# Kernel optimization log

Hardware: AMD Instinct MI355X
Metric: run time of the kernel (lower is better)

## Reference

```python
import jax, jax.numpy as jnp
import numpy as np

N, FIN, F, H = 4096, 128, 64, 8
NEG = -1e10


def setup_inputs() -> dict:
    key = jax.random.key(0)
    ks = jax.random.split(key, 6)
    X = jax.random.normal(ks[0], (N, FIN), dtype=jnp.float32)
    # sparse-ish binary adjacency with self loops, stored dense (as the layer expects)
    A = (jax.random.uniform(ks[1], (N, N)) < 0.05).astype(jnp.int32)
    A = A.at[jnp.arange(N), jnp.arange(N)].set(1)
    W = jax.random.normal(ks[2], (H, FIN, F), dtype=jnp.float32) * (1.0 / np.sqrt(FIN))
    b = jnp.zeros((H, F), dtype=jnp.float32)
    a_self = jax.random.normal(ks[3], (H, F), dtype=jnp.float32) * (1.0 / np.sqrt(F))
    a_neigh = jax.random.normal(ks[4], (H, F), dtype=jnp.float32) * (1.0 / np.sqrt(F))
    return {"X": X, "A": A, "W": W, "b": b, "a_self": a_self, "a_neigh": a_neigh}


def reference(X, A, W, b, a_self, a_neigh):
    # Dropout layers run in inference mode in the original call -> identity.
    feats = jnp.einsum('nf,hfo->hno', X, W)              # [H, N, F]
    s_self = jnp.einsum('hno,ho->hn', feats, a_self)     # [H, N]
    s_neigh = jnp.einsum('hno,ho->hn', feats, a_neigh)   # [H, N]
    scores = s_self[:, :, None] + s_neigh[:, None, :]    # [H, N, N]
    scores = jnp.where(scores > 0, scores, 0.2 * scores)  # LeakyReLU(0.2)
    mask = (1.0 - A.astype(jnp.float32)) * NEG            # [N, N]
    attn = jax.nn.softmax(scores + mask[None], axis=-1)   # [H, N, N]
    out = jnp.einsum('hnm,hmo->hno', attn, feats) + b[:, None, :]
    out = jax.nn.elu(out)                                 # [H, N, F]
    # concat heads -> [N, H*F]
    return jnp.transpose(out, (1, 0, 2)).reshape(N, H * F)
```

## Files before the change

kernel.cpp:

```cpp
#include <hip/hip_runtime.h>
#include <cmath>


#define NN 4096
#define FIN 128
#define FF 64
#define HH 8

typedef _Float16 h2 __attribute__((ext_vector_type(2)));
typedef _Float16 h4 __attribute__((ext_vector_type(4)));
typedef _Float16 h8 __attribute__((ext_vector_type(8)));
typedef float f32x2 __attribute__((ext_vector_type(2)));
typedef float f32x4 __attribute__((ext_vector_type(4)));

union H8 {
  h8 v;
  h2 p[4];
};
union H4 {
  h4 v;
  h2 p[2];
};

static __device__ __forceinline__ void gload16(const void* g, void* l) {
  __builtin_amdgcn_global_load_lds(
      (const __attribute__((address_space(1))) unsigned int*)g,
      (__attribute__((address_space(3))) unsigned int*)l, 16, 0, 0);
}

__global__ __launch_bounds__(256) void pack_kernel(
    const int* __restrict__ A, const float* __restrict__ W,
    const float* __restrict__ X, unsigned long long* __restrict__ bits,
    _Float16* __restrict__ Wsw, _Float16* __restrict__ Xsw) {
  const int b = blockIdx.x;
  const int tid = threadIdx.x;
  const int wave = tid >> 6, lane = tid & 63;
  if (b < NN) {
    __shared__ int ldsT[4][4][256];
    const int* ar = A + (size_t)b * NN;
    int4 v[4];
#pragma unroll
    for (int it = 0; it < 4; ++it) {
      const int g = wave * 4 + it;
      v[it] = *(const int4*)(ar + g * 256 + lane * 4);
    }
#pragma unroll
    for (int it = 0; it < 4; ++it) *(int4*)&ldsT[wave][it][lane * 4] = v[it];
    unsigned long long* br = bits + ((size_t)b << 6);
#pragma unroll
    for (int it = 0; it < 4; ++it) {
      const int g = wave * 4 + it;
      int w0 = ldsT[wave][it][0 * 64 + lane];
      int w1 = ldsT[wave][it][1 * 64 + lane];
      int w2 = ldsT[wave][it][2 * 64 + lane];
      int w3 = ldsT[wave][it][3 * 64 + lane];
      unsigned long long m0 = __ballot(w0 != 0);
      unsigned long long m1 = __ballot(w1 != 0);
      unsigned long long m2 = __ballot(w2 != 0);
      unsigned long long m3 = __ballot(w3 != 0);
      if (lane == 0) {
        ulonglong2 p0 = {m0, m1}, p1 = {m2, m3};
        *(ulonglong2*)(br + g * 4 + 0) = p0;
        *(ulonglong2*)(br + g * 4 + 2) = p1;
      }
    }
  } else if (b < NN + 2) {
    const int h0 = (b - NN) * 4;
    for (int h = h0; h < h0 + 4; ++h) {
      for (int c = tid; c < 1024; c += 256) {
        int ln = c & 63, nb = (c >> 6) & 3, kt = c >> 8;
        int f = nb * 16 + (ln & 15);
        int k0 = kt * 32 + (ln >> 4) * 8;
        h8 v;
#pragma unroll
        for (int j = 0; j < 8; ++j)
          v[j] = (_Float16)W[((size_t)(h * FIN) + k0 + j) * FF + f];
        *(h8*)(Wsw + ((size_t)(((h * 4 + kt) * 4 + nb) * 64 + ln)) * 8) = v;
      }
    }
  } else {
    const int tile = (b - NN - 2) * 4 + wave;
    const int l16 = lane & 15, quad = lane >> 4;
    const float* xr = X + (size_t)(tile * 16 + l16) * FIN;
#pragma unroll
    for (int kt = 0; kt < 4; ++kt) {
      int k0 = kt * 32 + quad * 8;
      f32x4 x0 = *(const f32x4*)(xr + k0);
      f32x4 x1 = *(const f32x4*)(xr + k0 + 4);
      h8 v = {(_Float16)x0[0], (_Float16)x0[1], (_Float16)x0[2],
              (_Float16)x0[3], (_Float16)x1[0], (_Float16)x1[1],
              (_Float16)x1[2], (_Float16)x1[3]};
      *(h8*)(Xsw + ((size_t)((tile * 4 + kt) * 64 + lane)) * 8) = v;
    }
  }
}

__global__ __launch_bounds__(256) void feats_kernel(
    const _Float16* __restrict__ Xsw, const _Float16* __restrict__ Wsw,
    const float* __restrict__ a_self, const float* __restrict__ a_neigh,
    _Float16* __restrict__ feats_sw, _Float16* __restrict__ es_h,
    _Float16* __restrict__ esn_h, _Float16* __restrict__ et_h,
    _Float16* __restrict__ etn_h) {
  const int h = blockIdx.y;
  const int tid = threadIdx.x, wave = tid >> 6, lane = tid & 63;
  const int l16 = lane & 15, quad = lane >> 4;
  const int rt = blockIdx.x * 4 + wave;
  const int r0 = rt * 16;

  f32x4 acc[4];
#pragma unroll
  for (int nb = 0; nb < 4; ++nb) acc[nb] = (f32x4){0.f, 0.f, 0.f, 0.f};

  const _Float16* xp = Xsw + ((size_t)(rt * 4) * 64 + lane) * 8;
  const _Float16* wp = Wsw + ((size_t)(h * 16) * 64 + lane) * 8;
  h8 Af[4];
#pragma unroll
  for (int kt = 0; kt < 4; ++kt) Af[kt] = *(const h8*)(xp + kt * 512);
#pragma unroll
  for (int kt = 0; kt < 4; ++kt)
#pragma unroll
    for (int nb = 0; nb < 4; ++nb) {
      h8 Bf = *(const h8*)(wp + (kt * 4 + nb) * 512);
      acc[nb] = __builtin_amdgcn_mfma_f32_16x16x32_f16(Af[kt], Bf, acc[nb], 0, 0, 0);
    }

  float as[4], an[4];
#pragma unroll
  for (int nb = 0; nb < 4; ++nb) {
    as[nb] = a_self[h * FF + nb * 16 + l16];
    an[nb] = a_neigh[h * FF + nb * 16 + l16];
  }
#pragma unroll
  for (int r = 0; r < 4; ++r) {
    float ps = acc[0][r] * as[0] + acc[1][r] * as[1] + acc[2][r] * as[2] +
               acc[3][r] * as[3];
    float pn = acc[0][r] * an[0] + acc[1][r] * an[1] + acc[2][r] * an[2] +
               acc[3][r] * an[3];
#pragma unroll
    for (int m = 1; m <= 8; m <<= 1) {
      ps += __shfl_xor(ps, m, 64);
      pn += __shfl_xor(pn, m, 64);
    }
    if (l16 == 0) {
      int node = h * NN + r0 + quad * 4 + r;
      es_h[node] = (_Float16)__expf(ps - 2.0f);
      esn_h[node] = (_Float16)__expf(0.2f * ps - 2.0f);
      et_h[node] = (_Float16)__expf(pn - 2.0f);
      etn_h[node] = (_Float16)__expf(0.2f * pn - 2.0f);
    }
  }

  const int kb = r0 >> 5;
  const int quadA = ((r0 >> 4) & 1) * 2 + (quad >> 1);
  const int jbase = (quad & 1) << 2;
#pragma unroll
  for (int nb = 0; nb < 4; ++nb) {
    h4 v = {(_Float16)acc[nb][0], (_Float16)acc[nb][1], (_Float16)acc[nb][2],
            (_Float16)acc[nb][3]};
    size_t off = ((size_t)((h * 128 + kb) * 4 + nb) << 9) +
                 ((quadA * 16 + l16) << 3) + jbase;
    *(h4*)(feats_sw + off) = v;
  }
}

__global__ __launch_bounds__(512, 4) void attn_kernel(
    const unsigned long long* __restrict__ Abits,
    const _Float16* __restrict__ feats_sw, const _Float16* __restrict__ es_h,
    const _Float16* __restrict__ esn_h, const _Float16* __restrict__ et_h,
    const _Float16* __restrict__ etn_h, const float* __restrict__ bias,
    float* __restrict__ out) {
  const int bid = blockIdx.x;
  const int h = bid & 7, n0 = (bid >> 3) << 6;
  const int tid = threadIdx.x, wave = tid >> 6, lane = tid & 63;
  const int l16 = lane & 15, quad = lane >> 4;
  const int rh = wave & 1, ctw = (wave >> 1) & 1, kfw = wave >> 2;
  const int shTot = (kfw << 5) + (quad << 3);

  __shared__ __align__(16) char smem[3 * 19456];
  __shared__ h4 lutS[16];

  if (tid < 16) {
    h4 m;
#pragma unroll
    for (int j = 0; j < 4; ++j) m[j] = (_Float16)((tid >> j) & 1);
    lutS[tid] = m;
  }
  __syncthreads();

  h2 esp[2], esnp[2];
#pragma unroll
  for (int rt = 0; rt < 2; ++rt) {
    const int myrow = n0 + (rh << 5) + (rt << 4) + l16;
    _Float16 e = es_h[h * NN + myrow];
    _Float16 en = esn_h[h * NN + myrow];
    esp[rt] = (h2){e, e};
    esnp[rt] = (h2){en, en};
  }

  f32x4 acc[2][4], accd[2];
#pragma unroll
  for (int rt = 0; rt < 2; ++rt) {
    accd[rt] = (f32x4){0.f, 0.f, 0.f, 0.f};
#pragma unroll
    for (int nb = 0; nb < 4; ++nb) acc[rt][nb] = (f32x4){0.f, 0.f, 0.f, 0.f};
  }
  const h8 ONES = {(_Float16)1.f, (_Float16)1.f, (_Float16)1.f, (_Float16)1.f,
                   (_Float16)1.f, (_Float16)1.f, (_Float16)1.f, (_Float16)1.f};

  const char* gF = (const char*)feats_sw + ((size_t)h << 19);
  const char* gE = (const char*)et_h + (h << 13);
  const char* gEN = (const char*)etn_h + (h << 13);
  const char* gB = (const char*)Abits + ((size_t)n0 << 9);

#define STAGE(s_, Lp_)                                                         \
  do {                                                                         \
    char* L_ = (char*)(Lp_);                                                   \
    const char* src_ = gF + ((size_t)(s_) << 14) + (wave << 11) + (lane << 4); \
    gload16(src_, L_ + (wave << 11) + (lane << 4));                            \
    gload16(src_ + 1024, L_ + (wave << 11) + 1024 + (lane << 4));              \
    if (wave == 0)                                                             \
      gload16(gE + ((s_) << 8) + (l16 << 4), L_ + 16384 + (lane << 4));        \
    if (wave == 1)                                                             \
      gload16(gEN + ((s_) << 8) + (l16 << 4), L_ + 17408 + (lane << 4));       \
    if (wave == 2)                                                             \
      gload16(gB + ((size_t)lane << 9) + ((s_) << 4), L_ + 18432 + (lane << 4)); \
  } while (0)

#define ITER(s_, SL, NSL, dostage_, last_)                                     \
  {                                                                            \
    __builtin_amdgcn_sched_barrier(0);                                         \
    if (last_) {                                                               \
      asm volatile("s_waitcnt vmcnt(0)" ::: "memory");                         \
    } else if (wave < 3) {                                                     \
      asm volatile("s_waitcnt vmcnt(3)" ::: "memory");                         \
    } else {                                                                   \
      asm volatile("s_waitcnt vmcnt(2)" ::: "memory");                         \
    }                                                                          \
    __builtin_amdgcn_sched_barrier(0);                                         \
    __builtin_amdgcn_s_barrier();                                              \
    if (dostage_) STAGE((s_) + 2, smem + (NSL)*19456);                         \
    const char* L = smem + (SL)*19456;                                         \
    unsigned long long mb0 = *(const unsigned long long*)(                     \
        L + 18432 + (((rh << 5) + l16) << 4) + (ctw << 3));                    \
    unsigned long long mb1 = *(const unsigned long long*)(                     \
        L + 18432 + (((rh << 5) + 16 + l16) << 4) + (ctw << 3));               \
    H8 ET, ETN;                                                                \
    ET.v = *(const h8*)(L + 16384 + (ctw << 7) + (kfw << 6) + (quad << 4));    \
    ETN.v = *(const h8*)(L + 17408 + (ctw << 7) + (kfw << 6) + (quad << 4));   \
    const char* fB = L + (ctw << 13) + (kfw << 12) + (lane << 4);              \
    h8 B0 = *(const h8*)(fB);                                                  \
    h8 B1 = *(const h8*)(fB + 1024);                                           \
    h8 B2 = *(const h8*)(fB + 2048);                                           \
    h8 B3 = *(const h8*)(fB + 3072);                                           \
    _Pragma("unroll") for (int rt = 0; rt < 2; ++rt) {                         \
      const unsigned byt = (unsigned)((rt ? mb1 : mb0) >> shTot) & 0xFFu;      \
      H4 mlo, mhi;                                                             \
      mlo.v = lutS[byt & 15u];                                                 \
      mhi.v = lutS[byt >> 4];                                                  \
      H8 P;                                                                    \
      _Pragma("unroll") for (int p = 0; p < 4; ++p) {                          \
        h2 a_ = esp[rt] * ET.p[p];                                             \
        h2 b_ = esnp[rt] * ETN.p[p];                                           \
        h2 r_ = __builtin_elementwise_max(a_, b_);                             \
        P.p[p] = r_ * (p < 2 ? mlo.p[p] : mhi.p[p - 2]);                       \
      }                                                                        \
      __builtin_amdgcn_s_setprio(1);                                           \
      acc[rt][0] =                                                             \
          __builtin_amdgcn_mfma_f32_16x16x32_f16(P.v, B0, acc[rt][0], 0, 0, 0);\
      acc[rt][1] =                                                             \
          __builtin_amdgcn_mfma_f32_16x16x32_f16(P.v, B1, acc[rt][1], 0, 0, 0);\
      acc[rt][2] =                                                             \
          __builtin_amdgcn_mfma_f32_16x16x32_f16(P.v, B2, acc[rt][2], 0, 0, 0);\
      acc[rt][3] =                                                             \
          __builtin_amdgcn_mfma_f32_16x16x32_f16(P.v, B3, acc[rt][3], 0, 0, 0);\
      accd[rt] =                                                               \
          __builtin_amdgcn_mfma_f32_16x16x32_f16(P.v, ONES, accd[rt], 0, 0, 0);\
      __builtin_amdgcn_s_setprio(0);                                           \
    }                                                                          \
  }

  STAGE(0, smem);
  STAGE(1, smem + 19456);

  for (int sb = 0; sb < 30; sb += 3) {
    ITER(sb + 0, 0, 2, 1, 0);
    ITER(sb + 1, 1, 0, 1, 0);
    ITER(sb + 2, 2, 1, 1, 0);
  }
  ITER(30, 0, 2, 0, 0);
  ITER(31, 1, 0, 0, 1);
#undef ITER
#undef STAGE

  float(*accL)[16][68] = (float(*)[16][68])smem;
  float* denL = (float*)(smem + 8 * 16 * 68 * 4);
  const int erow = tid >> 4;
  const int rh_o = erow >> 4, r16 = erow & 15;
  const int ec0 = (tid & 15) << 2;
#pragma unroll
  for (int rt = 0; rt < 2; ++rt) {
    __syncthreads();
#pragma unroll
    for (int nb = 0; nb < 4; ++nb)
#pragma unroll
      for (int r = 0; r < 4; ++r)
        accL[wave][quad * 4 + r][nb * 16 + l16] = acc[rt][nb][r];
    if (l16 == 0) {
#pragma unroll
      for (int r = 0; r < 4; ++r) denL[wave * 16 + quad * 4 + r] = accd[rt][r];
    }
    __syncthreads();
    f32x4 v = (f32x4){0.f, 0.f, 0.f, 0.f};
    float dn = 0.f;
#pragma unroll
    for (int cw = 0; cw < 4; ++cw) {
      const int w = rh_o + ((cw & 1) << 1) + ((cw >> 1) << 2);
      v += *(const f32x4*)&accL[w][r16][ec0];
      dn += denL[w * 16 + r16];
    }
    float inv = 1.0f / dn;
    const f32x4 bv = *(const f32x4*)(bias + h * FF + ec0);
#pragma unroll
    for (int i = 0; i < 4; ++i) {
      float x = v[i] * inv + bv[i];
      v[i] = x > 0.f ? x : (__expf(x) - 1.0f);
    }
    *(f32x4*)(out + (size_t)(n0 + (rh_o << 5) + (rt << 4) + r16) * (HH * FF) +
              h * FF + ec0) = v;
  }
}

extern "C" void kernel_launch(void* const* d_in, const int* in_sizes, int n_in,
                              void* d_out, int out_size, void* d_ws,
                              size_t ws_size, hipStream_t stream) {
  const float* X = (const float*)d_in[0];
  const int* A = (const int*)d_in[1];
  const float* W = (const float*)d_in[2];
  const float* b = (const float*)d_in[3];
  const float* a_self = (const float*)d_in[4];
  const float* a_neigh = (const float*)d_in[5];
  float* out = (float*)d_out;

  char* ws = (char*)d_ws;
  unsigned long long* Abits = (unsigned long long*)ws;
  _Float16* feats_sw = (_Float16*)(ws + (2u << 20));
  _Float16* es_h = (_Float16*)(ws + (6u << 20));
  _Float16* esn_h = (_Float16*)(ws + (6u << 20) + (64u << 10));
  _Float16* et_h = (_Float16*)(ws + (6u << 20) + (128u << 10));
  _Float16* etn_h = (_Float16*)(ws + (6u << 20) + (192u << 10));
  _Float16* Wsw = (_Float16*)(ws + (6u << 20) + (256u << 10));
  _Float16* Xsw = (_Float16*)(ws + (6u << 20) + (384u << 10));

  pack_kernel<<<NN + 66, 256, 0, stream>>>(A, W, X, Abits, Wsw, Xsw);
  feats_kernel<<<dim3(64, 8), 256, 0, stream>>>(Xsw, Wsw, a_self, a_neigh,
                                                feats_sw, es_h, esn_h, et_h,
                                                etn_h);
  attn_kernel<<<512, 512, 0, stream>>>(Abits, feats_sw, es_h, esn_h, et_h,
                                       etn_h, b, out);
}
```

Measured before the change: 142.0 us.

## Widen attention k-tile, give each wave all 64 rows, replace denominator MFMA with fdot2

The attention kernel now has each wave cover all 64 rows (four row tiles) over a quarter of the column chunk, and each stage doubles to 256 neighbour columns. So every B fragment loaded from LDS feeds four row tiles instead of two, with half as many iterations and barriers. The denominator MFMA against a ones vector is replaced by per-lane fdot2 accumulations plus cross-quad shuffles, removing one MFMA per row tile. The pipeline drops from triple to double buffering with a full vmcnt(0) wait each iteration, which may expose global load latency. The larger accumulator set also raises register pressure at 512 threads per block.

```diff
diff --git a/kernel.cpp b/kernel.cpp
--- a/kernel.cpp
+++ b/kernel.cpp
@@ -21,6 +21,15 @@
   h4 v;
   h2 p[2];
 };
+
+static __device__ __forceinline__ float dot2acc(h2 a, float c) {
+#if __has_builtin(__builtin_amdgcn_fdot2)
+  return __builtin_amdgcn_fdot2(a, (h2){(_Float16)1.f, (_Float16)1.f}, c,
+                                false);
+#else
+  return c + (float)a[0] + (float)a[1];
+#endif
+}
 
 static __device__ __forceinline__ void gload16(const void* g, void* l) {
   __builtin_amdgcn_global_load_lds(
@@ -173,10 +182,10 @@
   const int h = bid & 7, n0 = (bid >> 3) << 6;
   const int tid = threadIdx.x, wave = tid >> 6, lane = tid & 63;
   const int l16 = lane & 15, quad = lane >> 4;
-  const int rh = wave & 1, ctw = (wave >> 1) & 1, kfw = wave >> 2;
-  const int shTot = (kfw << 5) + (quad << 3);
-
-  __shared__ __align__(16) char smem[3 * 19456];
+  const int ctw = wave & 3, kfw = wave >> 2;
+  const int shq = quad << 3;
+
+  __shared__ __align__(16) char smem[2 * 36864];
   __shared__ h4 lutS[16];
 
   if (tid < 16) {
@@ -187,73 +196,70 @@
   }
   __syncthreads();
 
-  h2 esp[2], esnp[2];
-#pragma unroll
-  for (int rt = 0; rt < 2; ++rt) {
-    const int myrow = n0 + (rh << 5) + (rt << 4) + l16;
+  h2 esp[4], esnp[4];
+#pragma unroll
+  for (int rt = 0; rt < 4; ++rt) {
+    const int myrow = n0 + (rt << 4) + l16;
     _Float16 e = es_h[h * NN + myrow];
     _Float16 en = esn_h[h * NN + myrow];
     esp[rt] = (h2){e, e};
     esnp[rt] = (h2){en, en};
   }
 
-  f32x4 acc[2][4], accd[2];
-#pragma unroll
-  for (int rt = 0; rt < 2; ++rt) {
-    accd[rt] = (f32x4){0.f, 0.f, 0.f, 0.f};
+  f32x4 acc[4][4];
+  float dsA[4] = {0.f, 0.f, 0.f, 0.f}, dsB[4] = {0.f, 0.f, 0.f, 0.f};
+#pragma unroll
+  for (int rt = 0; rt < 4; ++rt)
 #pragma unroll
     for (int nb = 0; nb < 4; ++nb) acc[rt][nb] = (f32x4){0.f, 0.f, 0.f, 0.f};
-  }
-  const h8 ONES = {(_Float16)1.f, (_Float16)1.f, (_Float16)1.f, (_Float16)1.f,
-                   (_Float16)1.f, (_Float16)1.f, (_Float16)1.f, (_Float16)1.f};
 
   const char* gF = (const char*)feats_sw + ((size_t)h << 19);
   const char* gE = (const char*)et_h + (h << 13);
   const char* gEN = (const char*)etn_h + (h << 13);
   const char* gB = (const char*)Abits + ((size_t)n0 << 9);
 
+  const unsigned fO = (wave << 12) + (lane << 4);
+
 #define STAGE(s_, Lp_)                                                         \
   do {                                                                         \
     char* L_ = (char*)(Lp_);                                                   \
-    const char* src_ = gF + ((size_t)(s_) << 14) + (wave << 11) + (lane << 4); \
-    gload16(src_, L_ + (wave << 11) + (lane << 4));                            \
-    gload16(src_ + 1024, L_ + (wave << 11) + 1024 + (lane << 4));              \
+    const char* sf_ = gF + ((size_t)(s_) << 15) + fO;                          \
+    _Pragma("unroll") for (int i = 0; i < 4; ++i)                              \
+        gload16(sf_ + (i << 10), L_ + fO + (i << 10));                         \
     if (wave == 0)                                                             \
-      gload16(gE + ((s_) << 8) + (l16 << 4), L_ + 16384 + (lane << 4));        \
+      gload16(gE + ((s_) << 9) + (lane << 4), L_ + 32768 + (lane << 4));       \
     if (wave == 1)                                                             \
-      gload16(gEN + ((s_) << 8) + (l16 << 4), L_ + 17408 + (lane << 4));       \
+      gload16(gEN + ((s_) << 9) + (lane << 4), L_ + 33792 + (lane << 4));      \
     if (wave == 2)                                                             \
-      gload16(gB + ((size_t)lane << 9) + ((s_) << 4), L_ + 18432 + (lane << 4)); \
+      gload16(gB + ((size_t)(lane >> 1) << 9) + ((s_) << 5) +                  \
+                  ((lane & 1) << 4),                                           \
+              L_ + 34816 + (lane << 4));                                       \
+    if (wave == 3)                                                             \
+      gload16(gB + ((size_t)((lane >> 1) + 32) << 9) + ((s_) << 5) +           \
+                  ((lane & 1) << 4),                                           \
+              L_ + 35840 + (lane << 4));                                       \
   } while (0)
 
-#define ITER(s_, SL, NSL, dostage_, last_)                                     \
+#define ITER(s_, SL, dostage_)                                                 \
   {                                                                            \
     __builtin_amdgcn_sched_barrier(0);                                         \
-    if (last_) {                                                               \
-      asm volatile("s_waitcnt vmcnt(0)" ::: "memory");                         \
-    } else if (wave < 3) {                                                     \
-      asm volatile("s_waitcnt vmcnt(3)" ::: "memory");                         \
-    } else {                                                                   \
-      asm volatile("s_waitcnt vmcnt(2)" ::: "memory");                         \
-    }                                                                          \
+    asm volatile("s_waitcnt vmcnt(0)" ::: "memory");                           \
     __builtin_amdgcn_sched_barrier(0);                                         \
     __builtin_amdgcn_s_barrier();                                              \
-    if (dostage_) STAGE((s_) + 2, smem + (NSL)*19456);                         \
-    const char* L = smem + (SL)*19456;                                         \
-    unsigned long long mb0 = *(const unsigned long long*)(                     \
-        L + 18432 + (((rh << 5) + l16) << 4) + (ctw << 3));                    \
-    unsigned long long mb1 = *(const unsigned long long*)(                     \
-        L + 18432 + (((rh << 5) + 16 + l16) << 4) + (ctw << 3));               \
+    if (dostage_) STAGE((s_) + 1, smem + (1 - (SL)) * 36864);                  \
+    const char* L = smem + (SL)*36864;                                         \
     H8 ET, ETN;                                                                \
-    ET.v = *(const h8*)(L + 16384 + (ctw << 7) + (kfw << 6) + (quad << 4));    \
-    ETN.v = *(const h8*)(L + 17408 + (ctw << 7) + (kfw << 6) + (quad << 4));   \
+    ET.v = *(const h8*)(L + 32768 + (ctw << 7) + (kfw << 6) + (quad << 4));    \
+    ETN.v = *(const h8*)(L + 33792 + (ctw << 7) + (kfw << 6) + (quad << 4));   \
     const char* fB = L + (ctw << 13) + (kfw << 12) + (lane << 4);              \
     h8 B0 = *(const h8*)(fB);                                                  \
     h8 B1 = *(const h8*)(fB + 1024);                                           \
     h8 B2 = *(const h8*)(fB + 2048);                                           \
     h8 B3 = *(const h8*)(fB + 3072);                                           \
-    _Pragma("unroll") for (int rt = 0; rt < 2; ++rt) {                         \
-      const unsigned byt = (unsigned)((rt ? mb1 : mb0) >> shTot) & 0xFFu;      \
+    _Pragma("unroll") for (int rt = 0; rt < 4; ++rt) {                         \
+      const unsigned w32 = *(const unsigned*)(                                 \
+          L + 34816 + (((rt << 4) + l16) << 5) + (ctw << 3) + (kfw << 2));     \
+      const unsigned byt = (w32 >> shq) & 0xFFu;                               \
       H4 mlo, mhi;                                                             \
       mlo.v = lutS[byt & 15u];                                                 \
       mhi.v = lutS[byt >> 4];                                                  \
@@ -262,7 +268,12 @@
         h2 a_ = esp[rt] * ET.p[p];                                             \
         h2 b_ = esnp[rt] * ETN.p[p];                                           \
         h2 r_ = __builtin_elementwise_max(a_, b_);                             \
-        P.p[p] = r_ * (p < 2 ? mlo.p[p] : mhi.p[p - 2]);                       \
+        h2 pm_ = r_ * (p < 2 ? mlo.p[p] : mhi.p[p - 2]);                       \
+        P.p[p] = pm_;                                                          \
+        if (p & 1)                                                             \
+          dsB[rt] = dot2acc(pm_, dsB[rt]);                                     \
+        else                                                                   \
+          dsA[rt] = dot2acc(pm_, dsA[rt]);                                     \
       }                                                                        \
       __builtin_amdgcn_s_setprio(1);                                           \
       acc[rt][0] =                                                             \
@@ -273,60 +284,65 @@
           __builtin_amdgcn_mfma_f32_16x16x32_f16(P.v, B2, acc[rt][2], 0, 0, 0);\
       acc[rt][3] =                                                             \
           __builtin_amdgcn_mfma_f32_16x16x32_f16(P.v, B3, acc[rt][3], 0, 0, 0);\
-      accd[rt] =                                                               \
-          __builtin_amdgcn_mfma_f32_16x16x32_f16(P.v, ONES, accd[rt], 0, 0, 0);\
       __builtin_amdgcn_s_setprio(0);                                           \
     }                                                                          \
   }
 
   STAGE(0, smem);
-  STAGE(1, smem + 19456);
-
-  for (int sb = 0; sb < 30; sb += 3) {
-    ITER(sb + 0, 0, 2, 1, 0);
-    ITER(sb + 1, 1, 0, 1, 0);
-    ITER(sb + 2, 2, 1, 1, 0);
-  }
-  ITER(30, 0, 2, 0, 0);
-  ITER(31, 1, 0, 0, 1);
+
+  for (int sb = 0; sb < 14; sb += 2) {
+    ITER(sb + 0, 0, 1);
+    ITER(sb + 1, 1, 1);
+  }
+  ITER(14, 0, 1);
+  ITER(15, 1, 0);
 #undef ITER
 #undef STAGE
 
-  float(*accL)[16][68] = (float(*)[16][68])smem;
-  float* denL = (float*)(smem + 8 * 16 * 68 * 4);
-  const int erow = tid >> 4;
-  const int rh_o = erow >> 4, r16 = erow & 15;
-  const int ec0 = (tid & 15) << 2;
-#pragma unroll
-  for (int rt = 0; rt < 2; ++rt) {
+  float den[4];
+#pragma unroll
+  for (int rt = 0; rt < 4; ++rt) {
+    float d = dsA[rt] + dsB[rt];
+    d += __shfl_xor(d, 16, 64);
+    d += __shfl_xor(d, 32, 64);
+    den[rt] = d;
+  }
+
+  float(*accL)[32][68] = (float(*)[32][68])smem;
+  float* denL = (float*)(smem + 8 * 32 * 68 * 4);
+  const int rr = tid >> 4, ec0 = (tid & 15) << 2;
+  const f32x4 bv = *(const f32x4*)(bias + h * FF + ec0);
+#pragma unroll
+  for (int ph = 0; ph < 2; ++ph) {
     __syncthreads();
 #pragma unroll
-    for (int nb = 0; nb < 4; ++nb)
-#pragma unroll
-      for (int r = 0; r < 4; ++r)
-        accL[wave][quad * 4 + r][nb * 16 + l16] = acc[rt][nb][r];
-    if (l16 == 0) {
-#pragma unroll
-      for (int r = 0; r < 4; ++r) denL[wave * 16 + quad * 4 + r] = accd[rt][r];
+    for (int r2 = 0; r2 < 2; ++r2) {
+      const int rt = ph * 2 + r2;
+#pragma unroll
+      for (int nb = 0; nb < 4; ++nb)
+#pragma unroll
+        for (int r = 0; r < 4; ++r)
+          accL[wave][(r2 << 4) + (quad << 2) + r][(nb << 4) + l16] =
+              acc[rt][nb][r];
+      if (quad == 0) denL[(wave << 5) + (r2 << 4) + l16] = den[rt];
     }
     __syncthreads();
     f32x4 v = (f32x4){0.f, 0.f, 0.f, 0.f};
     float dn = 0.f;
 #pragma unroll
-    for (int cw = 0; cw < 4; ++cw) {
-      const int w = rh_o + ((cw & 1) << 1) + ((cw >> 1) << 2);
-      v += *(const f32x4*)&accL[w][r16][ec0];
-      dn += denL[w * 16 + r16];
+    for (int w = 0; w < 8; ++w) {
+      v += *(const f32x4*)&accL[w][rr][ec0];
+      dn += denL[(w << 5) + rr];
     }
     float inv = 1.0f / dn;
-    const f32x4 bv = *(const f32x4*)(bias + h * FF + ec0);
+    f32x4 o;
 #pragma unroll
     for (int i = 0; i < 4; ++i) {
       float x = v[i] * inv + bv[i];
-      v[i] = x > 0.f ? x : (__expf(x) - 1.0f);
-    }
-    *(f32x4*)(out + (size_t)(n0 + (rh_o << 5) + (rt << 4) + r16) * (HH * FF) +
-              h * FF + ec0) = v;
+      o[i] = x > 0.f ? x : (__expf(x) - 1.0f);
+    }
+    *(f32x4*)(out + (size_t)(n0 + (ph << 5) + rr) * (HH * FF) + h * FF + ec0) =
+        o;
   }
 }
 
```

Result: slower. 184.6 us (+30.0%).

## Double rows per attention block and compute softmax denominators with dot2

Applied to the files above, without the earlier changes.

Each attention block now handles 128 rows instead of 64, so every staged feats tile from LDS feeds twice as many MFMAs, and the grid is halved to 256 blocks. The denominator MFMA against a ones vector is replaced by fdot2 accumulation on the VALU plus cross-quad shuffles. The LUT-based mask expansion is replaced by bitfield-extract and perm masking. The cost is more accumulator registers (launch bounds lowered to 2 blocks per CU) and only 256 blocks, which may leave some of the GPU's CUs idle.

```diff
diff --git a/kernel.cpp b/kernel.cpp
--- a/kernel.cpp
+++ b/kernel.cpp
@@ -17,10 +17,31 @@
   h8 v;
   h2 p[4];
 };
-union H4 {
-  h4 v;
-  h2 p[2];
+union U2 {
+  h2 h;
+  unsigned u;
 };
+
+static __device__ __forceinline__ float dot2acc(h2 a, float c) {
+#if __has_builtin(__builtin_amdgcn_fdot2)
+  return __builtin_amdgcn_fdot2(a, (h2){(_Float16)1.f, (_Float16)1.f}, c,
+                                false);
+#else
+  return c + (float)a[0] + (float)a[1];
+#endif
+}
+
+static __device__ __forceinline__ unsigned mask2(unsigned w, int j) {
+#if __has_builtin(__builtin_amdgcn_sbfe) && __has_builtin(__builtin_amdgcn_perm)
+  int lo = __builtin_amdgcn_sbfe((int)w, j, 1);
+  int hi = __builtin_amdgcn_sbfe((int)w, j + 1, 1);
+  return __builtin_amdgcn_perm((unsigned)hi, (unsigned)lo, 0x05040100u);
+#else
+  int lo = ((int)(w << (31 - j))) >> 31;
+  int hi = ((int)(w << (30 - j))) >> 31;
+  return ((unsigned)lo & 0xFFFFu) | ((unsigned)hi << 16);
+#endif
+}
 
 static __device__ __forceinline__ void gload16(const void* g, void* l) {
   __builtin_amdgcn_global_load_lds(
@@ -163,49 +184,37 @@
   }
 }
 
-__global__ __launch_bounds__(512, 4) void attn_kernel(
+__global__ __launch_bounds__(512, 2) void attn_kernel(
     const unsigned long long* __restrict__ Abits,
     const _Float16* __restrict__ feats_sw, const _Float16* __restrict__ es_h,
     const _Float16* __restrict__ esn_h, const _Float16* __restrict__ et_h,
     const _Float16* __restrict__ etn_h, const float* __restrict__ bias,
     float* __restrict__ out) {
   const int bid = blockIdx.x;
-  const int h = bid & 7, n0 = (bid >> 3) << 6;
+  const int h = bid & 7, n0 = (bid >> 3) << 7;
   const int tid = threadIdx.x, wave = tid >> 6, lane = tid & 63;
   const int l16 = lane & 15, quad = lane >> 4;
   const int rh = wave & 1, ctw = (wave >> 1) & 1, kfw = wave >> 2;
-  const int shTot = (kfw << 5) + (quad << 3);
-
-  __shared__ __align__(16) char smem[3 * 19456];
-  __shared__ h4 lutS[16];
-
-  if (tid < 16) {
-    h4 m;
-#pragma unroll
-    for (int j = 0; j < 4; ++j) m[j] = (_Float16)((tid >> j) & 1);
-    lutS[tid] = m;
-  }
-  __syncthreads();
-
-  h2 esp[2], esnp[2];
-#pragma unroll
-  for (int rt = 0; rt < 2; ++rt) {
-    const int myrow = n0 + (rh << 5) + (rt << 4) + l16;
+  const int shq = quad << 3;
+
+  __shared__ __align__(16) char smem[3 * 20480];
+
+  h2 esp[4], esnp[4];
+#pragma unroll
+  for (int rt = 0; rt < 4; ++rt) {
+    const int myrow = n0 + (rh << 6) + (rt << 4) + l16;
     _Float16 e = es_h[h * NN + myrow];
     _Float16 en = esn_h[h * NN + myrow];
     esp[rt] = (h2){e, e};
     esnp[rt] = (h2){en, en};
   }
 
-  f32x4 acc[2][4], accd[2];
-#pragma unroll
-  for (int rt = 0; rt < 2; ++rt) {
-    accd[rt] = (f32x4){0.f, 0.f, 0.f, 0.f};
+  f32x4 acc[4][4];
+  float dsA[4] = {0.f, 0.f, 0.f, 0.f}, dsB[4] = {0.f, 0.f, 0.f, 0.f};
+#pragma unroll
+  for (int rt = 0; rt < 4; ++rt)
 #pragma unroll
     for (int nb = 0; nb < 4; ++nb) acc[rt][nb] = (f32x4){0.f, 0.f, 0.f, 0.f};
-  }
-  const h8 ONES = {(_Float16)1.f, (_Float16)1.f, (_Float16)1.f, (_Float16)1.f,
-                   (_Float16)1.f, (_Float16)1.f, (_Float16)1.f, (_Float16)1.f};
 
   const char* gF = (const char*)feats_sw + ((size_t)h << 19);
   const char* gE = (const char*)et_h + (h << 13);
@@ -224,6 +233,9 @@
       gload16(gEN + ((s_) << 8) + (l16 << 4), L_ + 17408 + (lane << 4));       \
     if (wave == 2)                                                             \
       gload16(gB + ((size_t)lane << 9) + ((s_) << 4), L_ + 18432 + (lane << 4)); \
+    if (wave == 3)                                                             \
+      gload16(gB + ((size_t)(64 + lane) << 9) + ((s_) << 4),                   \
+              L_ + 19456 + (lane << 4));                                       \
   } while (0)
 
 #define ITER(s_, SL, NSL, dostage_, last_)                                     \
@@ -231,19 +243,15 @@
     __builtin_amdgcn_sched_barrier(0);                                         \
     if (last_) {                                                               \
       asm volatile("s_waitcnt vmcnt(0)" ::: "memory");                         \
-    } else if (wave < 3) {                                                     \
+    } else if (wave < 4) {                                                     \
       asm volatile("s_waitcnt vmcnt(3)" ::: "memory");                         \
     } else {                                                                   \
       asm volatile("s_waitcnt vmcnt(2)" ::: "memory");                         \
     }                                                                          \
     __builtin_amdgcn_sched_barrier(0);                                         \
     __builtin_amdgcn_s_barrier();                                              \
-    if (dostage_) STAGE((s_) + 2, smem + (NSL)*19456);                         \
-    const char* L = smem + (SL)*19456;                                         \
-    unsigned long long mb0 = *(const unsigned long long*)(                     \
-        L + 18432 + (((rh << 5) + l16) << 4) + (ctw << 3));                    \
-    unsigned long long mb1 = *(const unsigned long long*)(                     \
-        L + 18432 + (((rh << 5) + 16 + l16) << 4) + (ctw << 3));               \
+    if (dostage_) STAGE((s_) + 2, smem + (NSL)*20480);                         \
+    const char* L = smem + (SL)*20480;                                         \
     H8 ET, ETN;                                                                \
     ET.v = *(const h8*)(L + 16384 + (ctw << 7) + (kfw << 6) + (quad << 4));    \
     ETN.v = *(const h8*)(L + 17408 + (ctw << 7) + (kfw << 6) + (quad << 4));   \
@@ -252,17 +260,24 @@
     h8 B1 = *(const h8*)(fB + 1024);                                           \
     h8 B2 = *(const h8*)(fB + 2048);                                           \
     h8 B3 = *(const h8*)(fB + 3072);                                           \
-    _Pragma("unroll") for (int rt = 0; rt < 2; ++rt) {                         \
-      const unsigned byt = (unsigned)((rt ? mb1 : mb0) >> shTot) & 0xFFu;      \
-      H4 mlo, mhi;                                                             \
-      mlo.v = lutS[byt & 15u];                                                 \
-      mhi.v = lutS[byt >> 4];                                                  \
+    _Pragma("unroll") for (int rt = 0; rt < 4; ++rt) {                         \
+      const unsigned w32 = *(const unsigned*)(                                 \
+          L + 18432 + (((rh << 6) + (rt << 4) + l16) << 4) + (ctw << 3) +      \
+          (kfw << 2));                                                         \
+      const unsigned ws = w32 >> shq;                                          \
       H8 P;                                                                    \
       _Pragma("unroll") for (int p = 0; p < 4; ++p) {                          \
         h2 a_ = esp[rt] * ET.p[p];                                             \
         h2 b_ = esnp[rt] * ETN.p[p];                                           \
         h2 r_ = __builtin_elementwise_max(a_, b_);                             \
-        P.p[p] = r_ * (p < 2 ? mlo.p[p] : mhi.p[p - 2]);                       \
+        U2 u_;                                                                 \
+        u_.h = r_;                                                             \
+        u_.u &= mask2(ws, 2 * p);                                              \
+        P.p[p] = u_.h;                                                         \
+        if (p & 1)                                                             \
+          dsB[rt] = dot2acc(u_.h, dsB[rt]);                                    \
+        else                                                                   \
+          dsA[rt] = dot2acc(u_.h, dsA[rt]);                                    \
       }                                                                        \
       __builtin_amdgcn_s_setprio(1);                                           \
       acc[rt][0] =                                                             \
@@ -273,14 +288,12 @@
           __builtin_amdgcn_mfma_f32_16x16x32_f16(P.v, B2, acc[rt][2], 0, 0, 0);\
       acc[rt][3] =                                                             \
           __builtin_amdgcn_mfma_f32_16x16x32_f16(P.v, B3, acc[rt][3], 0, 0, 0);\
-      accd[rt] =                                                               \
-          __builtin_amdgcn_mfma_f32_16x16x32_f16(P.v, ONES, accd[rt], 0, 0, 0);\
       __builtin_amdgcn_s_setprio(0);                                           \
     }                                                                          \
   }
 
   STAGE(0, smem);
-  STAGE(1, smem + 19456);
+  STAGE(1, smem + 20480);
 
   for (int sb = 0; sb < 30; sb += 3) {
     ITER(sb + 0, 0, 2, 1, 0);
@@ -292,23 +305,30 @@
 #undef ITER
 #undef STAGE
 
+  float den[4];
+#pragma unroll
+  for (int rt = 0; rt < 4; ++rt) {
+    float d = dsA[rt] + dsB[rt];
+    d += __shfl_xor(d, 16, 64);
+    d += __shfl_xor(d, 32, 64);
+    den[rt] = d;
+  }
+
   float(*accL)[16][68] = (float(*)[16][68])smem;
   float* denL = (float*)(smem + 8 * 16 * 68 * 4);
-  const int erow = tid >> 4;
-  const int rh_o = erow >> 4, r16 = erow & 15;
+  const int row32 = tid >> 4;
+  const int rh_o = row32 >> 4, r16 = row32 & 15;
   const int ec0 = (tid & 15) << 2;
-#pragma unroll
-  for (int rt = 0; rt < 2; ++rt) {
+  const f32x4 bv = *(const f32x4*)(bias + h * FF + ec0);
+#pragma unroll
+  for (int ph = 0; ph < 4; ++ph) {
     __syncthreads();
 #pragma unroll
     for (int nb = 0; nb < 4; ++nb)
 #pragma unroll
       for (int r = 0; r < 4; ++r)
-        accL[wave][quad * 4 + r][nb * 16 + l16] = acc[rt][nb][r];
-    if (l16 == 0) {
-#pragma unroll
-      for (int r = 0; r < 4; ++r) denL[wave * 16 + quad * 4 + r] = accd[rt][r];
-    }
+        accL[wave][quad * 4 + r][nb * 16 + l16] = acc[ph][nb][r];
+    if (quad == 0) denL[(wave << 4) + l16] = den[ph];
     __syncthreads();
     f32x4 v = (f32x4){0.f, 0.f, 0.f, 0.f};
     float dn = 0.f;
@@ -316,17 +336,17 @@
     for (int cw = 0; cw < 4; ++cw) {
       const int w = rh_o + ((cw & 1) << 1) + ((cw >> 1) << 2);
       v += *(const f32x4*)&accL[w][r16][ec0];
-      dn += denL[w * 16 + r16];
+      dn += denL[(w << 4) + r16];
     }
     float inv = 1.0f / dn;
-    const f32x4 bv = *(const f32x4*)(bias + h * FF + ec0);
+    f32x4 o;
 #pragma unroll
     for (int i = 0; i < 4; ++i) {
       float x = v[i] * inv + bv[i];
-      v[i] = x > 0.f ? x : (__expf(x) - 1.0f);
-    }
-    *(f32x4*)(out + (size_t)(n0 + (rh_o << 5) + (rt << 4) + r16) * (HH * FF) +
-              h * FF + ec0) = v;
+      o[i] = x > 0.f ? x : (__expf(x) - 1.0f);
+    }
+    *(f32x4*)(out + (size_t)(n0 + (rh_o << 6) + (ph << 4) + r16) * (HH * FF) +
+              h * FF + ec0) = o;
   }
 }
 
@@ -355,6 +375,6 @@
   feats_kernel<<<dim3(64, 8), 256, 0, stream>>>(Xsw, Wsw, a_self, a_neigh,
                                                 feats_sw, es_h, esn_h, et_h,
                                                 etn_h);
-  attn_kernel<<<512, 512, 0, stream>>>(Abits, feats_sw, es_h, esn_h, et_h,
+  attn_kernel<<<256, 512, 0, stream>>>(Abits, feats_sw, es_h, esn_h, et_h,
                                        etn_h, b, out);
 }
```

New measurement: 145.2 us. +2.2%, slower.

## Split adjacency bit-packing across pack and feats kernels to overlap work

Applied to the files above, without the earlier changes.

Adjacency bit-packing is split in two. The first kernel packs the first 2048 rows along with the W/X fp16 conversion, and the feats GEMM kernel packs the remaining 2048 rows in extra blocks. The aim is to hide the A-matrix read (which is bandwidth bound) behind the feats MFMA work and shorten the first kernel. An unused dot2acc helper is also added. Because feats blocks are scheduled first, the packing blocks may end up running largely after them anyway.

```diff
diff --git a/kernel.cpp b/kernel.cpp
--- a/kernel.cpp
+++ b/kernel.cpp
@@ -22,50 +22,65 @@
   h2 p[2];
 };
 
+static __device__ __forceinline__ float dot2acc(h2 a, float c) {
+#if __has_builtin(__builtin_amdgcn_fdot2)
+  return __builtin_amdgcn_fdot2(a, (h2){(_Float16)1.f, (_Float16)1.f}, c,
+                                false);
+#else
+  return c + (float)a[0] + (float)a[1];
+#endif
+}
+
 static __device__ __forceinline__ void gload16(const void* g, void* l) {
   __builtin_amdgcn_global_load_lds(
       (const __attribute__((address_space(1))) unsigned int*)g,
       (__attribute__((address_space(3))) unsigned int*)l, 16, 0, 0);
 }
 
-__global__ __launch_bounds__(256) void pack_kernel(
+static __device__ __forceinline__ void pack_row(const int* __restrict__ A,
+                                                unsigned long long* __restrict__
+                                                    bits,
+                                                int row, int tid) {
+  __shared__ int ldsT[4][4][256];
+  const int wave = tid >> 6, lane = tid & 63;
+  const int* ar = A + (size_t)row * NN;
+  int4 v[4];
+#pragma unroll
+  for (int it = 0; it < 4; ++it) {
+    const int g = wave * 4 + it;
+    v[it] = *(const int4*)(ar + g * 256 + lane * 4);
+  }
+#pragma unroll
+  for (int it = 0; it < 4; ++it) *(int4*)&ldsT[wave][it][lane * 4] = v[it];
+  unsigned long long* br = bits + ((size_t)row << 6);
+#pragma unroll
+  for (int it = 0; it < 4; ++it) {
+    const int g = wave * 4 + it;
+    int w0 = ldsT[wave][it][0 * 64 + lane];
+    int w1 = ldsT[wave][it][1 * 64 + lane];
+    int w2 = ldsT[wave][it][2 * 64 + lane];
+    int w3 = ldsT[wave][it][3 * 64 + lane];
+    unsigned long long m0 = __ballot(w0 != 0);
+    unsigned long long m1 = __ballot(w1 != 0);
+    unsigned long long m2 = __ballot(w2 != 0);
+    unsigned long long m3 = __ballot(w3 != 0);
+    if (lane == 0) {
+      ulonglong2 p0 = {m0, m1}, p1 = {m2, m3};
+      *(ulonglong2*)(br + g * 4 + 0) = p0;
+      *(ulonglong2*)(br + g * 4 + 2) = p1;
+    }
+  }
+}
+
+__global__ __launch_bounds__(256) void k1_kernel(
     const int* __restrict__ A, const float* __restrict__ W,
     const float* __restrict__ X, unsigned long long* __restrict__ bits,
     _Float16* __restrict__ Wsw, _Float16* __restrict__ Xsw) {
   const int b = blockIdx.x;
   const int tid = threadIdx.x;
   const int wave = tid >> 6, lane = tid & 63;
-  if (b < NN) {
-    __shared__ int ldsT[4][4][256];
-    const int* ar = A + (size_t)b * NN;
-    int4 v[4];
-#pragma unroll
-    for (int it = 0; it < 4; ++it) {
-      const int g = wave * 4 + it;
-      v[it] = *(const int4*)(ar + g * 256 + lane * 4);
-    }
-#pragma unroll
-    for (int it = 0; it < 4; ++it) *(int4*)&ldsT[wave][it][lane * 4] = v[it];
-    unsigned long long* br = bits + ((size_t)b << 6);
-#pragma unroll
-    for (int it = 0; it < 4; ++it) {
-      const int g = wave * 4 + it;
-      int w0 = ldsT[wave][it][0 * 64 + lane];
-      int w1 = ldsT[wave][it][1 * 64 + lane];
-      int w2 = ldsT[wave][it][2 * 64 + lane];
-      int w3 = ldsT[wave][it][3 * 64 + lane];
-      unsigned long long m0 = __ballot(w0 != 0);
-      unsigned long long m1 = __ballot(w1 != 0);
-      unsigned long long m2 = __ballot(w2 != 0);
-      unsigned long long m3 = __ballot(w3 != 0);
-      if (lane == 0) {
-        ulonglong2 p0 = {m0, m1}, p1 = {m2, m3};
-        *(ulonglong2*)(br + g * 4 + 0) = p0;
-        *(ulonglong2*)(br + g * 4 + 2) = p1;
-      }
-    }
-  } else if (b < NN + 2) {
-    const int h0 = (b - NN) * 4;
+  if (b < 2) {
+    const int h0 = b * 4;
     for (int h = h0; h < h0 + 4; ++h) {
       for (int c = tid; c < 1024; c += 256) {
         int ln = c & 63, nb = (c >> 6) & 3, kt = c >> 8;
@@ -78,8 +93,8 @@
         *(h8*)(Wsw + ((size_t)(((h * 4 + kt) * 4 + nb) * 64 + ln)) * 8) = v;
       }
     }
-  } else {
-    const int tile = (b - NN - 2) * 4 + wave;
+  } else if (b < 66) {
+    const int tile = (b - 2) * 4 + wave;
     const int l16 = lane & 15, quad = lane >> 4;
     const float* xr = X + (size_t)(tile * 16 + l16) * FIN;
 #pragma unroll
@@ -92,19 +107,27 @@
               (_Float16)x1[2], (_Float16)x1[3]};
       *(h8*)(Xsw + ((size_t)((tile * 4 + kt) * 64 + lane)) * 8) = v;
     }
-  }
-}
-
-__global__ __launch_bounds__(256) void feats_kernel(
+  } else {
+    pack_row(A, bits, b - 66, tid);
+  }
+}
+
+__global__ __launch_bounds__(256) void k2_kernel(
+    const int* __restrict__ A, unsigned long long* __restrict__ bits,
     const _Float16* __restrict__ Xsw, const _Float16* __restrict__ Wsw,
     const float* __restrict__ a_self, const float* __restrict__ a_neigh,
     _Float16* __restrict__ feats_sw, _Float16* __restrict__ es_h,
     _Float16* __restrict__ esn_h, _Float16* __restrict__ et_h,
     _Float16* __restrict__ etn_h) {
-  const int h = blockIdx.y;
+  const int b = blockIdx.x;
   const int tid = threadIdx.x, wave = tid >> 6, lane = tid & 63;
+  if (b >= 512) {
+    pack_row(A, bits, 2048 + (b - 512), tid);
+    return;
+  }
+  const int rb = b & 63, h = b >> 6;
   const int l16 = lane & 15, quad = lane >> 4;
-  const int rt = blockIdx.x * 4 + wave;
+  const int rt = rb * 4 + wave;
   const int r0 = rt * 16;
 
   f32x4 acc[4];
@@ -351,10 +374,10 @@
   _Float16* Wsw = (_Float16*)(ws + (6u << 20) + (256u << 10));
   _Float16* Xsw = (_Float16*)(ws + (6u << 20) + (384u << 10));
 
-  pack_kernel<<<NN + 66, 256, 0, stream>>>(A, W, X, Abits, Wsw, Xsw);
-  feats_kernel<<<dim3(64, 8), 256, 0, stream>>>(Xsw, Wsw, a_self, a_neigh,
-                                                feats_sw, es_h, esn_h, et_h,
-                                                etn_h);
+  k1_kernel<<<66 + 2048, 256, 0, stream>>>(A, W, X, Abits, Wsw, Xsw);
+  k2_kernel<<<512 + 2048, 256, 0, stream>>>(A, Abits, Xsw, Wsw, a_self,
+                                            a_neigh, feats_sw, es_h, esn_h,
+                                            et_h, etn_h);
   attn_kernel<<<512, 512, 0, stream>>>(Abits, feats_sw, es_h, esn_h, et_h,
                                        etn_h, b, out);
 }
```

Result: no change. 141.1 us, median of 2 (-0.6%).
